# Kernel optimization log

Measured on AMD Instinct MI355X. Metric: run time of the kernel, lower is better.

## Reference

```python
import jax, jax.numpy as jnp
import numpy as np


def setup_inputs() -> dict:
    key = jax.random.key(0)
    inputs = jax.random.normal(key, (8, 2048, 512), dtype=jnp.float32)
    return {"inputs": inputs}


def reference(inputs) -> jnp.ndarray:
    # score[b,i,j] = <x_i, x_j>  (no 1/sqrt(d) scaling in the original)
    score = jnp.einsum("bsd,btd->bst", inputs, inputs)  # [B,S,S]
    distribution = jax.nn.softmax(score, axis=-1)
    # output = distribution @ inputs
    return jnp.einsum("bst,btd->bsd", distribution, inputs)
```

## Files before the change

### kernel.cpp

```cpp
#include <hip/hip_runtime.h>
#include <hip/hip_bf16.h>

#define BATCH 8
#define SEQ   2048
#define DIM   512
#define QB    32
#define KB    64
#define NT    512
#define NKV   (SEQ / KB)

typedef __attribute__((ext_vector_type(8))) short short8;
typedef __attribute__((ext_vector_type(4))) float f32x4;
typedef __attribute__((ext_vector_type(4))) unsigned short ushort4v;

__device__ __forceinline__ unsigned short f2bf(float f) {
    union { float f; unsigned u; } v; v.f = f;
    return (unsigned short)((v.u + 0x7FFFu + ((v.u >> 16) & 1u)) >> 16);
}

__device__ __forceinline__ int swz(int kv) {
    return (8 * (kv & 7)) ^ (16 * ((kv >> 3) & 3)) ^ (64 * ((kv >> 3) & 1));
}

__global__ void to_bf16_kernel(const float* __restrict__ X,
                               unsigned short* __restrict__ Y, int n8) {
    const int i = blockIdx.x * blockDim.x + threadIdx.x;
    if (i >= n8) return;
    const float4 a = ((const float4*)X)[i * 2];
    const float4 b = ((const float4*)X)[i * 2 + 1];
    short8 h;
    h[0] = f2bf(a.x); h[1] = f2bf(a.y); h[2] = f2bf(a.z); h[3] = f2bf(a.w);
    h[4] = f2bf(b.x); h[5] = f2bf(b.y); h[6] = f2bf(b.z); h[7] = f2bf(b.w);
    ((short8*)Y)[i] = h;
}

__global__ __launch_bounds__(NT, 2)
void attn_fwd(const unsigned short* __restrict__ Xbf, float* __restrict__ O) {
    const int b   = blockIdx.x & 7;
    const int qt  = blockIdx.x >> 3;
    const int tid = threadIdx.x;
    const int lane = tid & 63;
    const int w    = tid >> 6;
    const int col  = lane & 15;
    const int kgrp = lane >> 4;

    __shared__ alignas(16) unsigned short Klds[KB * DIM];
    __shared__ alignas(16) float Sbuf[QB][KB + 4];
    __shared__ alignas(16) unsigned short Pfrag[2][2][64][8];
    __shared__ float m_s[QB], l_s[QB], fac_s[QB];

    const unsigned short* Xb = Xbf + (size_t)b * SEQ * DIM;

    const int qs = w >> 2;
    const int kc = w & 3;
    short8 qfrag[16];
    {
        const int qrow = qt * QB + qs * 16 + col;
        const unsigned short* qp = Xb + (size_t)qrow * DIM;
        #pragma unroll
        for (int ks = 0; ks < 16; ++ks)
            qfrag[ks] = *(const short8*)(qp + ks * 32 + kgrp * 8);
    }

    if (tid < QB) { m_s[tid] = -INFINITY; l_s[tid] = 0.f; }

    f32x4 oacc[2][4];
    #pragma unroll
    for (int i = 0; i < 2; ++i)
        #pragma unroll
        for (int j = 0; j < 4; ++j)
            oacc[i][j] = (f32x4){0.f, 0.f, 0.f, 0.f};

    for (int t = 0; t < NKV; ++t) {
        __syncthreads();
        {
            const unsigned short* kp = Xb + (size_t)(t * KB) * DIM;
            const int kv = tid >> 3;
            const unsigned short* src = kp + (size_t)kv * DIM + (tid & 7) * 8;
            unsigned short* dst = &Klds[kv * DIM];
            const int sw = swz(kv);
            #pragma unroll
            for (int i = 0; i < 8; ++i) {
                const int d0 = i * 64 + (tid & 7) * 8;
                *(short8*)(dst + (d0 ^ sw)) = *(const short8*)(src + i * 64);
            }
        }
        __syncthreads();

        {
            const int kvrow = kc * 16 + col;
            const unsigned short* kbase = &Klds[kvrow * DIM];
            const int sw = swz(kvrow);
            f32x4 sacc = (f32x4){0.f,0.f,0.f,0.f};
            #pragma unroll
            for (int ks = 0; ks < 16; ++ks) {
                short8 kfr = *(const short8*)(kbase + ((ks * 32 + kgrp * 8) ^ sw));
                sacc = __builtin_amdgcn_mfma_f32_16x16x32_bf16(qfrag[ks], kfr, sacc, 0, 0, 0);
            }
            #pragma unroll
            for (int r = 0; r < 4; ++r)
                Sbuf[qs * 16 + kgrp * 4 + r][kc * 16 + col] = sacc[r];
        }
        __syncthreads();

        {
            const int r = tid >> 4;
            const int c = tid & 15;
            float4 sa = *(const float4*)&Sbuf[r][c * 4];
            float mloc = fmaxf(fmaxf(sa.x, sa.y), fmaxf(sa.z, sa.w));
            mloc = fmaxf(mloc, __shfl_xor(mloc, 1));
            mloc = fmaxf(mloc, __shfl_xor(mloc, 2));
            mloc = fmaxf(mloc, __shfl_xor(mloc, 4));
            mloc = fmaxf(mloc, __shfl_xor(mloc, 8));
            const float mold = m_s[r];
            const float mnew = fmaxf(mold, mloc);
            const float fac  = __expf(mold - mnew);
            float p0 = __expf(sa.x - mnew), p1 = __expf(sa.y - mnew);
            float p2 = __expf(sa.z - mnew), p3 = __expf(sa.w - mnew);
            float lsum = (p0 + p1) + (p2 + p3);
            lsum += __shfl_xor(lsum, 1);
            lsum += __shfl_xor(lsum, 2);
            lsum += __shfl_xor(lsum, 4);
            lsum += __shfl_xor(lsum, 8);
            ushort4v p4;
            p4[0] = f2bf(p0); p4[1] = f2bf(p1); p4[2] = f2bf(p2); p4[3] = f2bf(p3);
            *(ushort4v*)&Pfrag[r >> 4][c >> 3][(r & 15) + 16 * ((c >> 1) & 3)][(c & 1) * 4] = p4;
            if (c == 0) {
                m_s[r] = mnew;
                fac_s[r] = fac;
                l_s[r] = l_s[r] * fac + lsum;
            }
        }
        __syncthreads();

        #pragma unroll
        for (int q2 = 0; q2 < 2; ++q2) {
            #pragma unroll
            for (int r = 0; r < 4; ++r) {
                const float f = fac_s[q2 * 16 + kgrp * 4 + r];
                #pragma unroll
                for (int dt = 0; dt < 4; ++dt) oacc[q2][dt][r] *= f;
            }
        }
        #pragma unroll
        for (int kc2 = 0; kc2 < 2; ++kc2) {
            const int kvb = kc2 * 32 + kgrp * 8;
            short8 afr[2];
            #pragma unroll
            for (int q2 = 0; q2 < 2; ++q2)
                afr[q2] = *(const short8*)&Pfrag[q2][kc2][lane][0];
            #pragma unroll
            for (int dt = 0; dt < 4; ++dt) {
                const int d = w * 64 + dt * 16 + col;
                short8 bfr;
                #pragma unroll
                for (int j = 0; j < 8; ++j) {
                    const int kv = kvb + j;
                    bfr[j] = (short)Klds[kv * DIM + (d ^ swz(kv))];
                }
                #pragma unroll
                for (int q2 = 0; q2 < 2; ++q2)
                    oacc[q2][dt] = __builtin_amdgcn_mfma_f32_16x16x32_bf16(afr[q2], bfr, oacc[q2][dt], 0, 0, 0);
            }
        }
    }

    #pragma unroll
    for (int q2 = 0; q2 < 2; ++q2) {
        #pragma unroll
        for (int r = 0; r < 4; ++r) {
            const int row = q2 * 16 + kgrp * 4 + r;
            const float inv = 1.f / l_s[row];
            float* op = O + ((size_t)b * SEQ + qt * QB + row) * DIM + w * 64 + col;
            #pragma unroll
            for (int dt = 0; dt < 4; ++dt)
                op[dt * 16] = oacc[q2][dt][r] * inv;
        }
    }
}

extern "C" void kernel_launch(void* const* d_in, const int* in_sizes, int n_in,
                              void* d_out, int out_size, void* d_ws, size_t ws_size,
                              hipStream_t stream) {
    const float* X = (const float*)d_in[0];
    float* Out = (float*)d_out;
    unsigned short* Xbf = (unsigned short*)d_ws;

    const int n8 = BATCH * SEQ * DIM / 8;
    hipLaunchKernelGGL(to_bf16_kernel, dim3(n8 / 256), dim3(256), 0, stream, X, Xbf, n8);

    dim3 grid(BATCH * (SEQ / QB));
    dim3 block(NT);
    hipLaunchKernelGGL(attn_fwd, grid, block, 0, stream, Xbf, Out);
}
```

Measured before the change: 179.6 us.

## Double-buffer K tiles in LDS with async global_load_lds prefetch

Replaces the synchronous register-staged copy of each K/V tile into LDS with direct global-to-LDS async loads (global_load_lds, 16 bytes per lane). The loads go into a second LDS buffer so the next tile is fetched while the current one is used for QK^T, softmax and PV. The swizzle is applied on the global source address so the LDS layout stays the same as before. The point is to hide global load latency and drop the register round-trip and one barrier per iteration. In exchange, the doubled K buffer pushes LDS use to about 139KB per block, which likely allows only one block per CU instead of the two the launch bounds target.

```diff
diff --git a/kernel.cpp b/kernel.cpp
--- a/kernel.cpp
+++ b/kernel.cpp
@@ -34,6 +34,22 @@
     ((short8*)Y)[i] = h;
 }
 
+__device__ __forceinline__ void stage_tile(const unsigned short* __restrict__ Xb,
+                                           unsigned short* klds_buf,
+                                           int t, int w, int lane) {
+    const unsigned short* kp = Xb + (size_t)(t * KB) * DIM;
+    #pragma unroll
+    for (int k = 0; k < 8; ++k) {
+        const int kv = k * 8 + w;
+        const int dsrc = (lane * 8) ^ swz(kv);
+        const unsigned short* g = kp + (size_t)kv * DIM + dsrc;
+        unsigned short* l = klds_buf + kv * DIM;
+        __builtin_amdgcn_global_load_lds(
+            (__attribute__((address_space(1))) void*)(g),
+            (__attribute__((address_space(3))) void*)(l), 16, 0, 0);
+    }
+}
+
 __global__ __launch_bounds__(NT, 2)
 void attn_fwd(const unsigned short* __restrict__ Xbf, float* __restrict__ O) {
     const int b   = blockIdx.x & 7;
@@ -44,7 +60,7 @@
     const int col  = lane & 15;
     const int kgrp = lane >> 4;
 
-    __shared__ alignas(16) unsigned short Klds[KB * DIM];
+    __shared__ alignas(16) unsigned short Klds[2][KB * DIM];
     __shared__ alignas(16) float Sbuf[QB][KB + 4];
     __shared__ alignas(16) unsigned short Pfrag[2][2][64][8];
     __shared__ float m_s[QB], l_s[QB], fac_s[QB];
@@ -71,25 +87,17 @@
         for (int j = 0; j < 4; ++j)
             oacc[i][j] = (f32x4){0.f, 0.f, 0.f, 0.f};
 
+    stage_tile(Xb, &Klds[0][0], 0, w, lane);
+    asm volatile("s_waitcnt vmcnt(0)" ::: "memory");
+    __syncthreads();
+
     for (int t = 0; t < NKV; ++t) {
-        __syncthreads();
-        {
-            const unsigned short* kp = Xb + (size_t)(t * KB) * DIM;
-            const int kv = tid >> 3;
-            const unsigned short* src = kp + (size_t)kv * DIM + (tid & 7) * 8;
-            unsigned short* dst = &Klds[kv * DIM];
-            const int sw = swz(kv);
-            #pragma unroll
-            for (int i = 0; i < 8; ++i) {
-                const int d0 = i * 64 + (tid & 7) * 8;
-                *(short8*)(dst + (d0 ^ sw)) = *(const short8*)(src + i * 64);
-            }
-        }
-        __syncthreads();
+        const int cur = t & 1;
+        if (t + 1 < NKV) stage_tile(Xb, &Klds[cur ^ 1][0], t + 1, w, lane);
 
         {
             const int kvrow = kc * 16 + col;
-            const unsigned short* kbase = &Klds[kvrow * DIM];
+            const unsigned short* kbase = &Klds[cur][kvrow * DIM];
             const int sw = swz(kvrow);
             f32x4 sacc = (f32x4){0.f,0.f,0.f,0.f};
             #pragma unroll
@@ -156,13 +164,16 @@
                 #pragma unroll
                 for (int j = 0; j < 8; ++j) {
                     const int kv = kvb + j;
-                    bfr[j] = (short)Klds[kv * DIM + (d ^ swz(kv))];
+                    bfr[j] = (short)Klds[cur][kv * DIM + (d ^ swz(kv))];
                 }
                 #pragma unroll
                 for (int q2 = 0; q2 < 2; ++q2)
                     oacc[q2][dt] = __builtin_amdgcn_mfma_f32_16x16x32_bf16(afr[q2], bfr, oacc[q2][dt], 0, 0, 0);
             }
         }
+
+        asm volatile("s_waitcnt vmcnt(0)" ::: "memory");
+        __syncthreads();
     }
 
     #pragma unroll
```

Measured after the change: 183.1 us. No clear change (+1.9%).

## Halve KV tile and split QK^T over head-dim halves to raise occupancy

Applied to the files above, without the earlier changes.

Shrinks the KV tile from 64 to 32 rows, which halves the K tile in LDS. The QK^T work is redistributed so each wave covers one 16x16 score block over half of the head dimension, with the two partial sums written to separate Sbuf slices and added during the softmax step. This halves the per-thread Q fragment registers and raises the launch-bounds occupancy hint from 2 to 4 blocks. In exchange there are twice as many KV iterations, each with four barriers, so per-tile synchronisation and softmax overhead per score grows.

```diff
diff --git a/kernel.cpp b/kernel.cpp
--- a/kernel.cpp
+++ b/kernel.cpp
@@ -5,13 +5,14 @@
 #define SEQ   2048
 #define DIM   512
 #define QB    32
-#define KB    64
+#define KB    32
 #define NT    512
 #define NKV   (SEQ / KB)
 
 typedef __attribute__((ext_vector_type(8))) short short8;
 typedef __attribute__((ext_vector_type(4))) float f32x4;
 typedef __attribute__((ext_vector_type(4))) unsigned short ushort4v;
+typedef __attribute__((ext_vector_type(2))) unsigned short ushort2v;
 
 __device__ __forceinline__ unsigned short f2bf(float f) {
     union { float f; unsigned u; } v; v.f = f;
@@ -34,7 +35,7 @@
     ((short8*)Y)[i] = h;
 }
 
-__global__ __launch_bounds__(NT, 2)
+__global__ __launch_bounds__(NT, 4)
 void attn_fwd(const unsigned short* __restrict__ Xbf, float* __restrict__ O) {
     const int b   = blockIdx.x & 7;
     const int qt  = blockIdx.x >> 3;
@@ -43,23 +44,24 @@
     const int w    = tid >> 6;
     const int col  = lane & 15;
     const int kgrp = lane >> 4;
+    const int qi = (w >> 1) & 1;
+    const int ki = w & 1;
+    const int dh = w >> 2;
 
     __shared__ alignas(16) unsigned short Klds[KB * DIM];
-    __shared__ alignas(16) float Sbuf[QB][KB + 4];
-    __shared__ alignas(16) unsigned short Pfrag[2][2][64][8];
+    __shared__ alignas(16) float Sbuf[2][QB][KB + 4];
+    __shared__ alignas(16) unsigned short Pfrag[2][64][8];
     __shared__ float m_s[QB], l_s[QB], fac_s[QB];
 
     const unsigned short* Xb = Xbf + (size_t)b * SEQ * DIM;
 
-    const int qs = w >> 2;
-    const int kc = w & 3;
-    short8 qfrag[16];
+    short8 qfrag[8];
     {
-        const int qrow = qt * QB + qs * 16 + col;
+        const int qrow = qt * QB + qi * 16 + col;
         const unsigned short* qp = Xb + (size_t)qrow * DIM;
         #pragma unroll
-        for (int ks = 0; ks < 16; ++ks)
-            qfrag[ks] = *(const short8*)(qp + ks * 32 + kgrp * 8);
+        for (int ks = 0; ks < 8; ++ks)
+            qfrag[ks] = *(const short8*)(qp + (dh * 8 + ks) * 32 + kgrp * 8);
     }
 
     if (tid < QB) { m_s[tid] = -INFINITY; l_s[tid] = 0.f; }
@@ -75,39 +77,42 @@
         __syncthreads();
         {
             const unsigned short* kp = Xb + (size_t)(t * KB) * DIM;
-            const int kv = tid >> 3;
-            const unsigned short* src = kp + (size_t)kv * DIM + (tid & 7) * 8;
+            const int kv = tid >> 4;
+            const unsigned short* src = kp + (size_t)kv * DIM + (tid & 15) * 8;
             unsigned short* dst = &Klds[kv * DIM];
             const int sw = swz(kv);
             #pragma unroll
-            for (int i = 0; i < 8; ++i) {
-                const int d0 = i * 64 + (tid & 7) * 8;
-                *(short8*)(dst + (d0 ^ sw)) = *(const short8*)(src + i * 64);
+            for (int i = 0; i < 4; ++i) {
+                const int d0 = i * 128 + (tid & 15) * 8;
+                *(short8*)(dst + (d0 ^ sw)) = *(const short8*)(src + i * 128);
             }
         }
         __syncthreads();
 
         {
-            const int kvrow = kc * 16 + col;
+            const int kvrow = ki * 16 + col;
             const unsigned short* kbase = &Klds[kvrow * DIM];
             const int sw = swz(kvrow);
             f32x4 sacc = (f32x4){0.f,0.f,0.f,0.f};
             #pragma unroll
-            for (int ks = 0; ks < 16; ++ks) {
-                short8 kfr = *(const short8*)(kbase + ((ks * 32 + kgrp * 8) ^ sw));
+            for (int ks = 0; ks < 8; ++ks) {
+                short8 kfr = *(const short8*)(kbase + (((dh * 8 + ks) * 32 + kgrp * 8) ^ sw));
                 sacc = __builtin_amdgcn_mfma_f32_16x16x32_bf16(qfrag[ks], kfr, sacc, 0, 0, 0);
             }
             #pragma unroll
             for (int r = 0; r < 4; ++r)
-                Sbuf[qs * 16 + kgrp * 4 + r][kc * 16 + col] = sacc[r];
+                Sbuf[dh][qi * 16 + kgrp * 4 + r][ki * 16 + col] = sacc[r];
         }
         __syncthreads();
 
         {
             const int r = tid >> 4;
             const int c = tid & 15;
-            float4 sa = *(const float4*)&Sbuf[r][c * 4];
-            float mloc = fmaxf(fmaxf(sa.x, sa.y), fmaxf(sa.z, sa.w));
+            float2 v0 = *(const float2*)&Sbuf[0][r][c * 2];
+            float2 v1 = *(const float2*)&Sbuf[1][r][c * 2];
+            const float s0 = v0.x + v1.x;
+            const float s1 = v0.y + v1.y;
+            float mloc = fmaxf(s0, s1);
             mloc = fmaxf(mloc, __shfl_xor(mloc, 1));
             mloc = fmaxf(mloc, __shfl_xor(mloc, 2));
             mloc = fmaxf(mloc, __shfl_xor(mloc, 4));
@@ -115,16 +120,16 @@
             const float mold = m_s[r];
             const float mnew = fmaxf(mold, mloc);
             const float fac  = __expf(mold - mnew);
-            float p0 = __expf(sa.x - mnew), p1 = __expf(sa.y - mnew);
-            float p2 = __expf(sa.z - mnew), p3 = __expf(sa.w - mnew);
-            float lsum = (p0 + p1) + (p2 + p3);
+            const float p0 = __expf(s0 - mnew);
+            const float p1 = __expf(s1 - mnew);
+            float lsum = p0 + p1;
             lsum += __shfl_xor(lsum, 1);
             lsum += __shfl_xor(lsum, 2);
             lsum += __shfl_xor(lsum, 4);
             lsum += __shfl_xor(lsum, 8);
-            ushort4v p4;
-            p4[0] = f2bf(p0); p4[1] = f2bf(p1); p4[2] = f2bf(p2); p4[3] = f2bf(p3);
-            *(ushort4v*)&Pfrag[r >> 4][c >> 3][(r & 15) + 16 * ((c >> 1) & 3)][(c & 1) * 4] = p4;
+            ushort2v pp;
+            pp[0] = f2bf(p0); pp[1] = f2bf(p1);
+            *(ushort2v*)&Pfrag[r >> 4][(r & 15) + 16 * (c >> 2)][2 * (c & 3)] = pp;
             if (c == 0) {
                 m_s[r] = mnew;
                 fac_s[r] = fac;
@@ -142,13 +147,12 @@
                 for (int dt = 0; dt < 4; ++dt) oacc[q2][dt][r] *= f;
             }
         }
-        #pragma unroll
-        for (int kc2 = 0; kc2 < 2; ++kc2) {
-            const int kvb = kc2 * 32 + kgrp * 8;
+        {
+            const int kvb = kgrp * 8;
             short8 afr[2];
             #pragma unroll
             for (int q2 = 0; q2 < 2; ++q2)
-                afr[q2] = *(const short8*)&Pfrag[q2][kc2][lane][0];
+                afr[q2] = *(const short8*)&Pfrag[q2][lane][0];
             #pragma unroll
             for (int dt = 0; dt < 4; ++dt) {
                 const int d = w * 64 + dt * 16 + col;
```

After: 230.0 us. +28.0%, slower.
